# Optimization experiments

Measured on AMD Instinct MI355X. Metric: run time of the kernel, lower is better.

Reference implementation:

```python
import jax, jax.numpy as jnp
import numpy as np

KERNEL = 7          # kernel_size
DIL = 1             # dilation
PAD = 3             # padding (same output size for k=7, d=1, s=1)
STRIDE = 1


def setup_inputs() -> dict:
    key = jax.random.key(0)
    x = jax.random.normal(key, (4, 256, 64, 64), dtype=jnp.float32)
    return {"x": x}


def reference(x):
    b, c, h, w = x.shape
    k2 = KERNEL * KERNEL
    # im2col / F.unfold equivalent: (b, c*k2, h_out, w_out), features ordered
    # (channel, kh, kw) exactly like torch.nn.functional.unfold.
    patches = jax.lax.conv_general_dilated_patches(
        x,
        filter_shape=(KERNEL, KERNEL),
        window_strides=(STRIDE, STRIDE),
        padding=[(PAD, PAD), (PAD, PAD)],
        rhs_dilation=(DIL, DIL),
    )
    ho, wo = patches.shape[2], patches.shape[3]
    p = patches.reshape(b, c, k2, ho, wo)          # (b, c, k2, h, w)
    center = p[:, :, k2 // 2]                      # (b, c, h, w) center of window
    # per-pixel similarity of each window element to the center, over channels
    sim = jnp.einsum('bckhw,bchw->bkhw', p, center)  # (b, k2, h, w)
    attn = jax.nn.softmax(sim, axis=1)               # softmax over window dim
    # weighted sum of window features
    out = jnp.einsum('bkhw,bckhw->bchw', attn, p)    # (b, c, h, w)
    return out
```

## Files before the change

### kernel.cpp

```cpp
#include <hip/hip_runtime.h>

typedef float f4 __attribute__((ext_vector_type(4)));
typedef _Float16 h2 __attribute__((ext_vector_type(2)));

#define Hdim 64
#define Wdim 64
#define Cdim 256
#define HW (Hdim * Wdim)

__device__ __forceinline__ float fdot2f(h2 a, h2 b, float c) {
#if __has_builtin(__builtin_amdgcn_fdot2)
    return __builtin_amdgcn_fdot2(a, b, c, false);
#else
    float d;
    asm("v_dot2_f32_f16 %0, %1, %2, %3" : "=v"(d) : "v"(a), "v"(b), "v"(c));
    return d;
#endif
}

__global__ __launch_bounds__(512) void pack_kernel(const float* __restrict__ x,
                                                   float* __restrict__ pw)
{
    const int tid = blockIdx.x * 512 + threadIdx.x;
    const int wq = tid & 15;
    const int h  = (tid >> 4) & 63;
    const int cp = (tid >> 10) & 127;
    const int b  = tid >> 17;
    const float* s0 = x + ((size_t)b * Cdim + 2 * cp) * HW + h * 64 + wq * 4;
    f4 v0 = *(const f4*)s0;
    f4 v1 = *(const f4*)(s0 + HW);
    f4 ov;
    #pragma unroll
    for (int p = 0; p < 4; ++p) {
        h2 o;
        o[0] = (_Float16)v0[p];
        o[1] = (_Float16)v1[p];
        ov[p] = __builtin_bit_cast(float, o);
    }
    *(f4*)(pw + ((size_t)b * 128 + cp) * HW + h * 64 + wq * 4) = ov;
}

__global__ __launch_bounds__(512, 2) void selfattn_f16(const float* __restrict__ pwf,
                                                       float* __restrict__ out)
{
    const int bid = blockIdx.x;
    const int k   = bid & 7;
    const int seq = bid >> 3;
    const int b   = k >> 1;
    const int h   = (k & 1) * 32 + (seq >> 1);
    const int wbase = (seq & 1) * 32;
    const int t = threadIdx.x;

    __shared__ float simRed[49][32];
    __shared__ __align__(16) h2 attnH[49][32];
    __shared__ float redBuf[7][32];
    __shared__ float psumBuf[7][32];

    const float* pw = pwf + (size_t)b * (128 * HW);

    {
        const int w4 = t & 7;
        const int cp = (t >> 3) & 7;
        const int dy = t >> 6;
        const int lw0 = w4 * 4;
        const int w0g = wbase + lw0;

        if (dy < 7) {
            float sim[7][4];
            #pragma unroll
            for (int dx = 0; dx < 7; ++dx)
                #pragma unroll
                for (int p = 0; p < 4; ++p) sim[dx][p] = 0.f;

            const int row = h + dy - 3;
            if (row >= 0 && row < Hdim) {
                const bool hasL = (w0g != 0);
                const bool hasR = (w0g != 60);
                const float* xr = pw + (size_t)cp * HW + row * 64;
                const float* xc = pw + (size_t)cp * HW + h   * 64;
                for (int i = 0; i < 16; ++i) {
                    float fw[12];
                    if (hasL) {
                        f4 v = *(const f4*)(xr + w0g - 4);
                        fw[0]=v.x; fw[1]=v.y; fw[2]=v.z; fw[3]=v.w;
                    } else { fw[0]=0.f; fw[1]=0.f; fw[2]=0.f; fw[3]=0.f; }
                    {
                        f4 v = *(const f4*)(xr + w0g);
                        fw[4]=v.x; fw[5]=v.y; fw[6]=v.z; fw[7]=v.w;
                    }
                    if (hasR) {
                        f4 v = *(const f4*)(xr + w0g + 4);
                        fw[8]=v.x; fw[9]=v.y; fw[10]=v.z; fw[11]=v.w;
                    } else { fw[8]=0.f; fw[9]=0.f; fw[10]=0.f; fw[11]=0.f; }
                    f4 cen = *(const f4*)(xc + w0g);
                    h2 f2[12], cen2[4];
                    #pragma unroll
                    for (int j = 0; j < 12; ++j) f2[j] = __builtin_bit_cast(h2, fw[j]);
                    #pragma unroll
                    for (int p = 0; p < 4; ++p) cen2[p] = __builtin_bit_cast(h2, cen[p]);
                    #pragma unroll
                    for (int dx = 0; dx < 7; ++dx)
                        #pragma unroll
                        for (int p = 0; p < 4; ++p)
                            sim[dx][p] = fdot2f(cen2[p], f2[dx + p + 1], sim[dx][p]);
                    xr += 8 * HW;
                    xc += 8 * HW;
                }
            }
            #pragma unroll
            for (int dx = 0; dx < 7; ++dx)
                #pragma unroll
                for (int p = 0; p < 4; ++p) {
                    float v = sim[dx][p];
                    v += __shfl_xor(v, 8);
                    v += __shfl_xor(v, 16);
                    v += __shfl_xor(v, 32);
                    sim[dx][p] = v;
                }
            if (cp == 0) {
                #pragma unroll
                for (int dx = 0; dx < 7; ++dx)
                    *(f4*)&simRed[dy * 7 + dx][lw0] = *(const f4*)sim[dx];
            }
        }
    }
    __syncthreads();

    {
        const int w  = t & 31;
        const int kc = t >> 5;
        float sred[7], e[7];
        if (kc < 7) {
            float lmax = -3.0e38f;
            #pragma unroll
            for (int jj = 0; jj < 7; ++jj) {
                float s = simRed[kc * 7 + jj][w];
                sred[jj] = s;
                lmax = fmaxf(lmax, s);
            }
            redBuf[kc][w] = lmax;
        }
        __syncthreads();
        if (kc < 7) {
            float m = redBuf[0][w];
            #pragma unroll
            for (int q = 1; q < 7; ++q) m = fmaxf(m, redBuf[q][w]);
            float ps = 0.f;
            #pragma unroll
            for (int jj = 0; jj < 7; ++jj) {
                e[jj] = __expf(sred[jj] - m);
                ps += e[jj];
            }
            psumBuf[kc][w] = ps;
        }
        __syncthreads();
        if (kc < 7) {
            float l = psumBuf[0][w];
            #pragma unroll
            for (int q = 1; q < 7; ++q) l += psumBuf[q][w];
            float rinv = 1.0f / l;
            #pragma unroll
            for (int jj = 0; jj < 7; ++jj) {
                _Float16 ah = (_Float16)(e[jj] * rinv);
                h2 av; av[0] = ah; av[1] = ah;
                attnH[kc * 7 + jj][w] = av;
            }
        }
    }
    __syncthreads();

    {
        const int w4 = t & 7;
        const int ci = t >> 3;
        const int lw0 = w4 * 4;
        const int w0g = wbase + lw0;
        const bool hasL = (w0g != 0);
        const bool hasR = (w0g != 60);

        h2 acc2[2][4];
        #pragma unroll
        for (int pr = 0; pr < 2; ++pr)
            #pragma unroll
            for (int p = 0; p < 4; ++p) { acc2[pr][p][0] = (_Float16)0; acc2[pr][p][1] = (_Float16)0; }

        for (int dy = 0; dy < 7; ++dy) {
            const int row = h + dy - 3;
            if (row < 0 || row >= Hdim) continue;
            h2 a2[7][4];
            #pragma unroll
            for (int dx = 0; dx < 7; ++dx) {
                f4 v = *(const f4*)&attnH[dy * 7 + dx][lw0];
                #pragma unroll
                for (int p = 0; p < 4; ++p) a2[dx][p] = __builtin_bit_cast(h2, v[p]);
            }
            #pragma unroll
            for (int pr = 0; pr < 2; ++pr) {
                const float* xr = pw + (size_t)(2 * ci + pr) * HW + row * 64;
                float fw[12];
                if (hasL) {
                    f4 v = *(const f4*)(xr + w0g - 4);
                    fw[0]=v.x; fw[1]=v.y; fw[2]=v.z; fw[3]=v.w;
                } else { fw[0]=0.f; fw[1]=0.f; fw[2]=0.f; fw[3]=0.f; }
                {
                    f4 v = *(const f4*)(xr + w0g);
                    fw[4]=v.x; fw[5]=v.y; fw[6]=v.z; fw[7]=v.w;
                }
                if (hasR) {
                    f4 v = *(const f4*)(xr + w0g + 4);
                    fw[8]=v.x; fw[9]=v.y; fw[10]=v.z; fw[11]=v.w;
                } else { fw[8]=0.f; fw[9]=0.f; fw[10]=0.f; fw[11]=0.f; }
                h2 f2[12];
                #pragma unroll
                for (int j = 0; j < 12; ++j) f2[j] = __builtin_bit_cast(h2, fw[j]);
                #pragma unroll
                for (int dx = 0; dx < 7; ++dx)
                    #pragma unroll
                    for (int p = 0; p < 4; ++p)
                        acc2[pr][p] += a2[dx][p] * f2[dx + p + 1];
            }
        }

        float* ob = out + (size_t)b * (Cdim * HW) + h * Wdim + w0g;
        #pragma unroll
        for (int pr = 0; pr < 2; ++pr) {
            f4 o0, o1;
            #pragma unroll
            for (int p = 0; p < 4; ++p) {
                o0[p] = (float)acc2[pr][p][0];
                o1[p] = (float)acc2[pr][p][1];
            }
            const int c0 = 4 * ci + 2 * pr;
            *(f4*)(ob + (size_t)c0 * HW)       = o0;
            *(f4*)(ob + (size_t)(c0 + 1) * HW) = o1;
        }
    }
}

__global__ __launch_bounds__(512, 2) void selfattn_fb(const float* __restrict__ x,
                                                      float* __restrict__ out)
{
    const int bid = blockIdx.x;
    const int k   = bid & 7;
    const int seq = bid >> 3;
    const int b   = k >> 1;
    const int h   = (k & 1) * 32 + (seq >> 1);
    const int wbase = (seq & 1) * 32;
    const int t = threadIdx.x;

    __shared__ float simRed[49][32];
    __shared__ float attnBuf[49][32];
    __shared__ float redBuf[7][32];
    __shared__ float psumBuf[7][32];

    const float* xb = x + (size_t)b * (Cdim * HW);

    {
        const int w4 = t & 7;
        const int cp = (t >> 3) & 7;
        const int dy = t >> 6;
        const int lw0 = w4 * 4;
        const int w0g = wbase + lw0;

        if (dy < 7) {
            float sim[7][4];
            #pragma unroll
            for (int dx = 0; dx < 7; ++dx)
                #pragma unroll
                for (int p = 0; p < 4; ++p) sim[dx][p] = 0.f;

            const int row = h + dy - 3;
            if (row >= 0 && row < Hdim) {
                const bool hasL = (w0g != 0);
                const bool hasR = (w0g != 60);
                const float* xrA = xb + (size_t)cp * HW + row * Wdim;
                const float* xcA = xb + (size_t)cp * HW + h   * Wdim;
                const float* xrB = xrA + (size_t)128 * HW;
                const float* xcB = xcA + (size_t)128 * HW;
                #pragma unroll 2
                for (int i = 0; i < 16; ++i) {
                    float fA[12], fB[12];
                    if (hasL) {
                        f4 v = *(const f4*)(xrA + w0g - 4);
                        fA[0]=v.x; fA[1]=v.y; fA[2]=v.z; fA[3]=v.w;
                    } else { fA[0]=0.f; fA[1]=0.f; fA[2]=0.f; fA[3]=0.f; }
                    {
                        f4 v = *(const f4*)(xrA + w0g);
                        fA[4]=v.x; fA[5]=v.y; fA[6]=v.z; fA[7]=v.w;
                    }
                    if (hasR) {
                        f4 v = *(const f4*)(xrA + w0g + 4);
                        fA[8]=v.x; fA[9]=v.y; fA[10]=v.z; fA[11]=v.w;
                    } else { fA[8]=0.f; fA[9]=0.f; fA[10]=0.f; fA[11]=0.f; }
                    if (hasL) {
                        f4 v = *(const f4*)(xrB + w0g - 4);
                        fB[0]=v.x; fB[1]=v.y; fB[2]=v.z; fB[3]=v.w;
                    } else { fB[0]=0.f; fB[1]=0.f; fB[2]=0.f; fB[3]=0.f; }
                    {
                        f4 v = *(const f4*)(xrB + w0g);
                        fB[4]=v.x; fB[5]=v.y; fB[6]=v.z; fB[7]=v.w;
                    }
                    if (hasR) {
                        f4 v = *(const f4*)(xrB + w0g + 4);
                        fB[8]=v.x; fB[9]=v.y; fB[10]=v.z; fB[11]=v.w;
                    } else { fB[8]=0.f; fB[9]=0.f; fB[10]=0.f; fB[11]=0.f; }
                    f4 cenA = *(const f4*)(xcA + w0g);
                    f4 cenB = *(const f4*)(xcB + w0g);
                    #pragma unroll
                    for (int dx = 0; dx < 7; ++dx)
                        #pragma unroll
                        for (int p = 0; p < 4; ++p)
                            sim[dx][p] += cenA[p] * fA[dx + p + 1]
                                        + cenB[p] * fB[dx + p + 1];
                    xrA += 8 * HW;  xcA += 8 * HW;
                    xrB += 8 * HW;  xcB += 8 * HW;
                }
            }
            #pragma unroll
            for (int dx = 0; dx < 7; ++dx)
                #pragma unroll
                for (int p = 0; p < 4; ++p) {
                    float v = sim[dx][p];
                    v += __shfl_xor(v, 8);
                    v += __shfl_xor(v, 16);
                    v += __shfl_xor(v, 32);
                    sim[dx][p] = v;
                }
            if (cp == 0) {
                #pragma unroll
                for (int dx = 0; dx < 7; ++dx)
                    *(f4*)&simRed[dy * 7 + dx][lw0] = *(const f4*)sim[dx];
            }
        }
    }
    __syncthreads();

    {
        const int w  = t & 31;
        const int kc = t >> 5;
        float sred[7], e[7];
        if (kc < 7) {
            float lmax = -3.0e38f;
            #pragma unroll
            for (int jj = 0; jj < 7; ++jj) {
                float s = simRed[kc * 7 + jj][w];
                sred[jj] = s;
                lmax = fmaxf(lmax, s);
            }
            redBuf[kc][w] = lmax;
        }
        __syncthreads();
        if (kc < 7) {
            float m = redBuf[0][w];
            #pragma unroll
            for (int q = 1; q < 7; ++q) m = fmaxf(m, redBuf[q][w]);
            float ps = 0.f;
            #pragma unroll
            for (int jj = 0; jj < 7; ++jj) {
                e[jj] = __expf(sred[jj] - m);
                ps += e[jj];
            }
            psumBuf[kc][w] = ps;
        }
        __syncthreads();
        if (kc < 7) {
            float l = psumBuf[0][w];
            #pragma unroll
            for (int q = 1; q < 7; ++q) l += psumBuf[q][w];
            float rinv = 1.0f / l;
            #pragma unroll
            for (int jj = 0; jj < 7; ++jj)
                attnBuf[kc * 7 + jj][w] = e[jj] * rinv;
        }
    }
    __syncthreads();

    {
        const int w4 = t & 7;
        const int ci = t >> 3;
        const int lw0 = w4 * 4;
        const int w0g = wbase + lw0;
        const int c0 = ci * 4;
        const bool hasL = (w0g != 0);
        const bool hasR = (w0g != 60);

        float acc[4][4];
        #pragma unroll
        for (int ch = 0; ch < 4; ++ch)
            #pragma unroll
            for (int p = 0; p < 4; ++p) acc[ch][p] = 0.f;

        for (int dy = 0; dy < 7; ++dy) {
            const int row = h + dy - 3;
            if (row < 0 || row >= Hdim) continue;
            float a[7][4];
            #pragma unroll
            for (int dx = 0; dx < 7; ++dx) {
                f4 v = *(const f4*)&attnBuf[dy * 7 + dx][lw0];
                a[dx][0]=v.x; a[dx][1]=v.y; a[dx][2]=v.z; a[dx][3]=v.w;
            }
            const float* xr = xb + (size_t)c0 * HW + row * Wdim;
            #pragma unroll
            for (int ch = 0; ch < 4; ++ch) {
                float fw[12];
                if (hasL) {
                    f4 v = *(const f4*)(xr + w0g - 4);
                    fw[0]=v.x; fw[1]=v.y; fw[2]=v.z; fw[3]=v.w;
                } else { fw[0]=0.f; fw[1]=0.f; fw[2]=0.f; fw[3]=0.f; }
                {
                    f4 v = *(const f4*)(xr + w0g);
                    fw[4]=v.x; fw[5]=v.y; fw[6]=v.z; fw[7]=v.w;
                }
                if (hasR) {
                    f4 v = *(const f4*)(xr + w0g + 4);
                    fw[8]=v.x; fw[9]=v.y; fw[10]=v.z; fw[11]=v.w;
                } else { fw[8]=0.f; fw[9]=0.f; fw[10]=0.f; fw[11]=0.f; }
                #pragma unroll
                for (int dx = 0; dx < 7; ++dx)
                    #pragma unroll
                    for (int p = 0; p < 4; ++p)
                        acc[ch][p] += a[dx][p] * fw[dx + p + 1];
                xr += HW;
            }
        }

        float* ob = out + (size_t)b * (Cdim * HW) + h * Wdim + wbase;
        #pragma unroll
        for (int ch = 0; ch < 4; ++ch)
            *(f4*)(ob + (size_t)(c0 + ch) * HW + lw0) = *(const f4*)acc[ch];
    }
}

extern "C" void kernel_launch(void* const* d_in, const int* in_sizes, int n_in,
                              void* d_out, int out_size, void* d_ws, size_t ws_size,
                              hipStream_t stream)
{
    const float* x = (const float*)d_in[0];
    float* out = (float*)d_out;
    const size_t need = (size_t)4 * 128 * HW * 4;
    if (ws_size >= need) {
        float* pw = (float*)d_ws;
        pack_kernel<<<dim3(1024), 512, 0, stream>>>(x, pw);
        selfattn_f16<<<dim3(512), 512, 0, stream>>>(pw, out);
    } else {
        selfattn_fb<<<dim3(512), 512, 0, stream>>>(x, out);
    }
}
```

Baseline: 33.21 us.

## Process two output rows per block to reuse shared neighbor rows

Each block now handles a pair of adjacent output rows with 1024 threads instead of one row with 512. The 8 input rows covering both 7-row windows are loaded once and used for both rows' similarity and weighted-sum stages. This roughly halves the redundant global loads of neighboring rows. Channels are split across two wave groups, and their partial sums are combined in shared memory. In exchange the grid shrinks to 256 blocks, which lowers the number of blocks per CU, and register pressure rises from the dual accumulators.

```diff
diff --git a/kernel.cpp b/kernel.cpp
--- a/kernel.cpp
+++ b/kernel.cpp
@@ -40,162 +40,54 @@
     *(f4*)(pw + ((size_t)b * 128 + cp) * HW + h * 64 + wq * 4) = ov;
 }
 
-__global__ __launch_bounds__(512, 2) void selfattn_f16(const float* __restrict__ pwf,
+__global__ __launch_bounds__(1024) void selfattn_hpair(const float* __restrict__ pwf,
                                                        float* __restrict__ out)
 {
     const int bid = blockIdx.x;
     const int k   = bid & 7;
     const int seq = bid >> 3;
     const int b   = k >> 1;
-    const int h   = (k & 1) * 32 + (seq >> 1);
+    const int hh  = k & 1;
+    const int hp  = seq >> 1;
+    const int h0  = hh * 32 + hp * 2;
+    const int h1  = h0 + 1;
     const int wbase = (seq & 1) * 32;
     const int t = threadIdx.x;
 
-    __shared__ float simRed[49][32];
-    __shared__ __align__(16) h2 attnH[49][32];
-    __shared__ float redBuf[7][32];
-    __shared__ float psumBuf[7][32];
+    __shared__ float simPart[2][2][49][32];
+    __shared__ __align__(16) h2 attnH[2][49][32];
+    __shared__ float redBuf[2][7][32];
+    __shared__ float psumBuf[2][7][32];
 
     const float* pw = pwf + (size_t)b * (128 * HW);
 
     {
+        const int wave = t >> 6;
+        const int r    = wave & 7;
+        const int g    = wave >> 3;
         const int w4 = t & 7;
         const int cp = (t >> 3) & 7;
-        const int dy = t >> 6;
         const int lw0 = w4 * 4;
         const int w0g = wbase + lw0;
-
-        if (dy < 7) {
-            float sim[7][4];
-            #pragma unroll
-            for (int dx = 0; dx < 7; ++dx)
-                #pragma unroll
-                for (int p = 0; p < 4; ++p) sim[dx][p] = 0.f;
-
-            const int row = h + dy - 3;
-            if (row >= 0 && row < Hdim) {
-                const bool hasL = (w0g != 0);
-                const bool hasR = (w0g != 60);
-                const float* xr = pw + (size_t)cp * HW + row * 64;
-                const float* xc = pw + (size_t)cp * HW + h   * 64;
-                for (int i = 0; i < 16; ++i) {
-                    float fw[12];
-                    if (hasL) {
-                        f4 v = *(const f4*)(xr + w0g - 4);
-                        fw[0]=v.x; fw[1]=v.y; fw[2]=v.z; fw[3]=v.w;
-                    } else { fw[0]=0.f; fw[1]=0.f; fw[2]=0.f; fw[3]=0.f; }
-                    {
-                        f4 v = *(const f4*)(xr + w0g);
-                        fw[4]=v.x; fw[5]=v.y; fw[6]=v.z; fw[7]=v.w;
-                    }
-                    if (hasR) {
-                        f4 v = *(const f4*)(xr + w0g + 4);
-                        fw[8]=v.x; fw[9]=v.y; fw[10]=v.z; fw[11]=v.w;
-                    } else { fw[8]=0.f; fw[9]=0.f; fw[10]=0.f; fw[11]=0.f; }
-                    f4 cen = *(const f4*)(xc + w0g);
-                    h2 f2[12], cen2[4];
-                    #pragma unroll
-                    for (int j = 0; j < 12; ++j) f2[j] = __builtin_bit_cast(h2, fw[j]);
-                    #pragma unroll
-                    for (int p = 0; p < 4; ++p) cen2[p] = __builtin_bit_cast(h2, cen[p]);
-                    #pragma unroll
-                    for (int dx = 0; dx < 7; ++dx)
-                        #pragma unroll
-                        for (int p = 0; p < 4; ++p)
-                            sim[dx][p] = fdot2f(cen2[p], f2[dx + p + 1], sim[dx][p]);
-                    xr += 8 * HW;
-                    xc += 8 * HW;
-                }
-            }
-            #pragma unroll
-            for (int dx = 0; dx < 7; ++dx)
-                #pragma unroll
-                for (int p = 0; p < 4; ++p) {
-                    float v = sim[dx][p];
-                    v += __shfl_xor(v, 8);
-                    v += __shfl_xor(v, 16);
-                    v += __shfl_xor(v, 32);
-                    sim[dx][p] = v;
-                }
-            if (cp == 0) {
-                #pragma unroll
-                for (int dx = 0; dx < 7; ++dx)
-                    *(f4*)&simRed[dy * 7 + dx][lw0] = *(const f4*)sim[dx];
-            }
-        }
-    }
-    __syncthreads();
-
-    {
-        const int w  = t & 31;
-        const int kc = t >> 5;
-        float sred[7], e[7];
-        if (kc < 7) {
-            float lmax = -3.0e38f;
-            #pragma unroll
-            for (int jj = 0; jj < 7; ++jj) {
-                float s = simRed[kc * 7 + jj][w];
-                sred[jj] = s;
-                lmax = fmaxf(lmax, s);
-            }
-            redBuf[kc][w] = lmax;
-        }
-        __syncthreads();
-        if (kc < 7) {
-            float m = redBuf[0][w];
-            #pragma unroll
-            for (int q = 1; q < 7; ++q) m = fmaxf(m, redBuf[q][w]);
-            float ps = 0.f;
-            #pragma unroll
-            for (int jj = 0; jj < 7; ++jj) {
-                e[jj] = __expf(sred[jj] - m);
-                ps += e[jj];
-            }
-            psumBuf[kc][w] = ps;
-        }
-        __syncthreads();
-        if (kc < 7) {
-            float l = psumBuf[0][w];
-            #pragma unroll
-            for (int q = 1; q < 7; ++q) l += psumBuf[q][w];
-            float rinv = 1.0f / l;
-            #pragma unroll
-            for (int jj = 0; jj < 7; ++jj) {
-                _Float16 ah = (_Float16)(e[jj] * rinv);
-                h2 av; av[0] = ah; av[1] = ah;
-                attnH[kc * 7 + jj][w] = av;
-            }
-        }
-    }
-    __syncthreads();
-
-    {
-        const int w4 = t & 7;
-        const int ci = t >> 3;
-        const int lw0 = w4 * 4;
-        const int w0g = wbase + lw0;
-        const bool hasL = (w0g != 0);
-        const bool hasR = (w0g != 60);
-
-        h2 acc2[2][4];
+        const int gr = h0 - 3 + r;
+        const bool grok = (gr >= 0 && gr < Hdim);
+        const bool use0 = (r <= 6);
+        const bool use1 = (r >= 1);
+
+        float sim0[7][4], sim1[7][4];
         #pragma unroll
-        for (int pr = 0; pr < 2; ++pr)
-            #pragma unroll
-            for (int p = 0; p < 4; ++p) { acc2[pr][p][0] = (_Float16)0; acc2[pr][p][1] = (_Float16)0; }
-
-        for (int dy = 0; dy < 7; ++dy) {
-            const int row = h + dy - 3;
-            if (row < 0 || row >= Hdim) continue;
-            h2 a2[7][4];
-            #pragma unroll
-            for (int dx = 0; dx < 7; ++dx) {
-                f4 v = *(const f4*)&attnH[dy * 7 + dx][lw0];
-                #pragma unroll
-                for (int p = 0; p < 4; ++p) a2[dx][p] = __builtin_bit_cast(h2, v[p]);
-            }
-            #pragma unroll
-            for (int pr = 0; pr < 2; ++pr) {
-                const float* xr = pw + (size_t)(2 * ci + pr) * HW + row * 64;
+        for (int dx = 0; dx < 7; ++dx)
+            #pragma unroll
+            for (int p = 0; p < 4; ++p) { sim0[dx][p] = 0.f; sim1[dx][p] = 0.f; }
+
+        if (grok) {
+            const bool hasL = (w0g != 0);
+            const bool hasR = (w0g != 60);
+            const float* xr  = pw + (size_t)(g * 8 + cp) * HW + gr * 64;
+            const float* xc0 = pw + (size_t)(g * 8 + cp) * HW + h0 * 64;
+            const float* xc1 = xc0 + 64;
+            #pragma unroll 2
+            for (int i = 0; i < 8; ++i) {
                 float fw[12];
                 if (hasL) {
                     f4 v = *(const f4*)(xr + w0g - 4);
@@ -211,28 +103,189 @@
                 } else { fw[8]=0.f; fw[9]=0.f; fw[10]=0.f; fw[11]=0.f; }
                 h2 f2[12];
                 #pragma unroll
-                for (int j = 0; j < 12; ++j) f2[j] = __builtin_bit_cast(h2, fw[j]);
+                for (int jj = 0; jj < 12; ++jj) f2[jj] = __builtin_bit_cast(h2, fw[jj]);
+                if (use0) {
+                    f4 c0 = *(const f4*)(xc0 + w0g);
+                    h2 c02[4];
+                    #pragma unroll
+                    for (int p = 0; p < 4; ++p) c02[p] = __builtin_bit_cast(h2, c0[p]);
+                    #pragma unroll
+                    for (int dx = 0; dx < 7; ++dx)
+                        #pragma unroll
+                        for (int p = 0; p < 4; ++p)
+                            sim0[dx][p] = fdot2f(c02[p], f2[dx + p + 1], sim0[dx][p]);
+                }
+                if (use1) {
+                    f4 c1 = *(const f4*)(xc1 + w0g);
+                    h2 c12[4];
+                    #pragma unroll
+                    for (int p = 0; p < 4; ++p) c12[p] = __builtin_bit_cast(h2, c1[p]);
+                    #pragma unroll
+                    for (int dx = 0; dx < 7; ++dx)
+                        #pragma unroll
+                        for (int p = 0; p < 4; ++p)
+                            sim1[dx][p] = fdot2f(c12[p], f2[dx + p + 1], sim1[dx][p]);
+                }
+                xr  += 16 * HW;
+                xc0 += 16 * HW;
+                xc1 += 16 * HW;
+            }
+        }
+        if (use0) {
+            #pragma unroll
+            for (int dx = 0; dx < 7; ++dx)
+                #pragma unroll
+                for (int p = 0; p < 4; ++p) {
+                    float v = sim0[dx][p];
+                    v += __shfl_xor(v, 8);
+                    v += __shfl_xor(v, 16);
+                    v += __shfl_xor(v, 32);
+                    sim0[dx][p] = v;
+                }
+        }
+        if (use1) {
+            #pragma unroll
+            for (int dx = 0; dx < 7; ++dx)
+                #pragma unroll
+                for (int p = 0; p < 4; ++p) {
+                    float v = sim1[dx][p];
+                    v += __shfl_xor(v, 8);
+                    v += __shfl_xor(v, 16);
+                    v += __shfl_xor(v, 32);
+                    sim1[dx][p] = v;
+                }
+        }
+        if (cp == 0) {
+            if (use0) {
                 #pragma unroll
                 for (int dx = 0; dx < 7; ++dx)
+                    *(f4*)&simPart[0][g][r * 7 + dx][lw0] = *(const f4*)sim0[dx];
+            }
+            if (use1) {
+                #pragma unroll
+                for (int dx = 0; dx < 7; ++dx)
+                    *(f4*)&simPart[1][g][(r - 1) * 7 + dx][lw0] = *(const f4*)sim1[dx];
+            }
+        }
+    }
+    __syncthreads();
+
+    {
+        const int hsel = t >> 9;
+        const int tt = t & 511;
+        const int w  = tt & 31;
+        const int kc = tt >> 5;
+        float sred[7], e[7];
+        if (kc < 7) {
+            float lmax = -3.0e38f;
+            #pragma unroll
+            for (int jj = 0; jj < 7; ++jj) {
+                const int idx = kc * 7 + jj;
+                float s = simPart[hsel][0][idx][w] + simPart[hsel][1][idx][w];
+                sred[jj] = s;
+                lmax = fmaxf(lmax, s);
+            }
+            redBuf[hsel][kc][w] = lmax;
+        }
+        __syncthreads();
+        if (kc < 7) {
+            float m = redBuf[hsel][0][w];
+            #pragma unroll
+            for (int q = 1; q < 7; ++q) m = fmaxf(m, redBuf[hsel][q][w]);
+            float ps = 0.f;
+            #pragma unroll
+            for (int jj = 0; jj < 7; ++jj) {
+                e[jj] = __expf(sred[jj] - m);
+                ps += e[jj];
+            }
+            psumBuf[hsel][kc][w] = ps;
+        }
+        __syncthreads();
+        if (kc < 7) {
+            float l = psumBuf[hsel][0][w];
+            #pragma unroll
+            for (int q = 1; q < 7; ++q) l += psumBuf[hsel][q][w];
+            float rinv = 1.0f / l;
+            #pragma unroll
+            for (int jj = 0; jj < 7; ++jj) {
+                _Float16 ah = (_Float16)(e[jj] * rinv);
+                h2 av; av[0] = ah; av[1] = ah;
+                attnH[hsel][kc * 7 + jj][w] = av;
+            }
+        }
+    }
+    __syncthreads();
+
+    {
+        const int w4 = t & 7;
+        const int ci = t >> 3;
+        const int lw0 = w4 * 4;
+        const int w0g = wbase + lw0;
+        const bool hasL = (w0g != 0);
+        const bool hasR = (w0g != 60);
+
+        h2 acc0[4], acc1[4];
+        #pragma unroll
+        for (int p = 0; p < 4; ++p) {
+            acc0[p][0] = (_Float16)0; acc0[p][1] = (_Float16)0;
+            acc1[p][0] = (_Float16)0; acc1[p][1] = (_Float16)0;
+        }
+
+        const float* xbase = pw + (size_t)ci * HW;
+        #pragma unroll 2
+        for (int rr = 0; rr < 8; ++rr) {
+            const int grow = h0 - 3 + rr;
+            if (grow < 0 || grow >= Hdim) continue;
+            const float* xr = xbase + grow * 64;
+            float fw[12];
+            if (hasL) {
+                f4 v = *(const f4*)(xr + w0g - 4);
+                fw[0]=v.x; fw[1]=v.y; fw[2]=v.z; fw[3]=v.w;
+            } else { fw[0]=0.f; fw[1]=0.f; fw[2]=0.f; fw[3]=0.f; }
+            {
+                f4 v = *(const f4*)(xr + w0g);
+                fw[4]=v.x; fw[5]=v.y; fw[6]=v.z; fw[7]=v.w;
+            }
+            if (hasR) {
+                f4 v = *(const f4*)(xr + w0g + 4);
+                fw[8]=v.x; fw[9]=v.y; fw[10]=v.z; fw[11]=v.w;
+            } else { fw[8]=0.f; fw[9]=0.f; fw[10]=0.f; fw[11]=0.f; }
+            h2 f2[12];
+            #pragma unroll
+            for (int jj = 0; jj < 12; ++jj) f2[jj] = __builtin_bit_cast(h2, fw[jj]);
+            if (rr <= 6) {
+                #pragma unroll
+                for (int dx = 0; dx < 7; ++dx) {
+                    f4 av = *(const f4*)&attnH[0][rr * 7 + dx][lw0];
                     #pragma unroll
                     for (int p = 0; p < 4; ++p)
-                        acc2[pr][p] += a2[dx][p] * f2[dx + p + 1];
-            }
-        }
-
-        float* ob = out + (size_t)b * (Cdim * HW) + h * Wdim + w0g;
+                        acc0[p] += __builtin_bit_cast(h2, av[p]) * f2[dx + p + 1];
+                }
+            }
+            if (rr >= 1) {
+                #pragma unroll
+                for (int dx = 0; dx < 7; ++dx) {
+                    f4 av = *(const f4*)&attnH[1][(rr - 1) * 7 + dx][lw0];
+                    #pragma unroll
+                    for (int p = 0; p < 4; ++p)
+                        acc1[p] += __builtin_bit_cast(h2, av[p]) * f2[dx + p + 1];
+                }
+            }
+        }
+
+        float* ob = out + (size_t)b * (Cdim * HW) + w0g;
+        f4 o00, o01, o10, o11;
         #pragma unroll
-        for (int pr = 0; pr < 2; ++pr) {
-            f4 o0, o1;
-            #pragma unroll
-            for (int p = 0; p < 4; ++p) {
-                o0[p] = (float)acc2[pr][p][0];
-                o1[p] = (float)acc2[pr][p][1];
-            }
-            const int c0 = 4 * ci + 2 * pr;
-            *(f4*)(ob + (size_t)c0 * HW)       = o0;
-            *(f4*)(ob + (size_t)(c0 + 1) * HW) = o1;
-        }
+        for (int p = 0; p < 4; ++p) {
+            o00[p] = (float)acc0[p][0];
+            o01[p] = (float)acc0[p][1];
+            o10[p] = (float)acc1[p][0];
+            o11[p] = (float)acc1[p][1];
+        }
+        *(f4*)(ob + (size_t)(2 * ci) * HW     + h0 * 64) = o00;
+        *(f4*)(ob + (size_t)(2 * ci + 1) * HW + h0 * 64) = o01;
+        *(f4*)(ob + (size_t)(2 * ci) * HW     + h1 * 64) = o10;
+        *(f4*)(ob + (size_t)(2 * ci + 1) * HW + h1 * 64) = o11;
     }
 }
 
@@ -440,7 +493,7 @@
     if (ws_size >= need) {
         float* pw = (float*)d_ws;
         pack_kernel<<<dim3(1024), 512, 0, stream>>>(x, pw);
-        selfattn_f16<<<dim3(512), 512, 0, stream>>>(pw, out);
+        selfattn_hpair<<<dim3(256), 1024, 0, stream>>>(pw, out);
     } else {
         selfattn_fb<<<dim3(512), 512, 0, stream>>>(x, out);
     }
```

Result: slower. 34.58 us (+4.1%).

## Split fused attention kernel into similarity and output kernels with global attn buffer

Applied to the files above, without the earlier changes.

The fused f16 kernel is split into two launches. ka_sim computes the 49-tap softmax weights and writes them to a workspace buffer. kb_out reloads them into LDS and computes the weighted sum over half the channel pairs per block, doubling the grid to 1024 blocks. The goal is more parallelism and lower register pressure in the output phase, at the cost of an extra launch, a global round-trip for the weights, and redundant halo loads across the two channel halves.

```diff
diff --git a/kernel.cpp b/kernel.cpp
--- a/kernel.cpp
+++ b/kernel.cpp
@@ -40,19 +40,19 @@
     *(f4*)(pw + ((size_t)b * 128 + cp) * HW + h * 64 + wq * 4) = ov;
 }
 
-__global__ __launch_bounds__(512, 2) void selfattn_f16(const float* __restrict__ pwf,
-                                                       float* __restrict__ out)
+__global__ __launch_bounds__(512, 2) void ka_sim(const float* __restrict__ pwf,
+                                                 float* __restrict__ attnG)
 {
     const int bid = blockIdx.x;
     const int k   = bid & 7;
     const int seq = bid >> 3;
     const int b   = k >> 1;
     const int h   = (k & 1) * 32 + (seq >> 1);
-    const int wbase = (seq & 1) * 32;
+    const int whalf = seq & 1;
+    const int wbase = whalf * 32;
     const int t = threadIdx.x;
 
     __shared__ float simRed[49][32];
-    __shared__ __align__(16) h2 attnH[49][32];
     __shared__ float redBuf[7][32];
     __shared__ float psumBuf[7][32];
 
@@ -159,12 +159,41 @@
             #pragma unroll
             for (int q = 1; q < 7; ++q) l += psumBuf[q][w];
             float rinv = 1.0f / l;
+            float* ag = attnG + (size_t)(((b * 64 + h) * 2 + whalf) * 49) * 32;
             #pragma unroll
             for (int jj = 0; jj < 7; ++jj) {
                 _Float16 ah = (_Float16)(e[jj] * rinv);
                 h2 av; av[0] = ah; av[1] = ah;
-                attnH[kc * 7 + jj][w] = av;
-            }
+                ag[(kc * 7 + jj) * 32 + w] = __builtin_bit_cast(float, av);
+            }
+        }
+    }
+}
+
+__global__ __launch_bounds__(512) void kb_out(const float* __restrict__ pwf,
+                                              const float* __restrict__ attnG,
+                                              float* __restrict__ out)
+{
+    const int bid = blockIdx.x;
+    const int k   = bid & 7;
+    const int seq = bid >> 3;
+    const int b   = k >> 1;
+    const int h   = (k & 1) * 32 + (seq >> 2);
+    const int whalf = (seq >> 1) & 1;
+    const int chalf = seq & 1;
+    const int wbase = whalf * 32;
+    const int t = threadIdx.x;
+
+    __shared__ __align__(16) h2 attnH[49][32];
+
+    const float* pw = pwf + (size_t)b * (128 * HW);
+
+    {
+        const float* ag = attnG + (size_t)(((b * 64 + h) * 2 + whalf) * 49) * 32;
+        if (t < 392) {
+            const int kk = t >> 3;
+            const int wq = t & 7;
+            *(f4*)&attnH[kk][wq * 4] = *(const f4*)(ag + kk * 32 + wq * 4);
         }
     }
     __syncthreads();
@@ -172,16 +201,15 @@
     {
         const int w4 = t & 7;
         const int ci = t >> 3;
+        const int pair = chalf * 64 + ci;
         const int lw0 = w4 * 4;
         const int w0g = wbase + lw0;
         const bool hasL = (w0g != 0);
         const bool hasR = (w0g != 60);
 
-        h2 acc2[2][4];
+        h2 acc2[4];
         #pragma unroll
-        for (int pr = 0; pr < 2; ++pr)
-            #pragma unroll
-            for (int p = 0; p < 4; ++p) { acc2[pr][p][0] = (_Float16)0; acc2[pr][p][1] = (_Float16)0; }
+        for (int p = 0; p < 4; ++p) { acc2[p][0] = (_Float16)0; acc2[p][1] = (_Float16)0; }
 
         for (int dy = 0; dy < 7; ++dy) {
             const int row = h + dy - 3;
@@ -193,46 +221,39 @@
                 #pragma unroll
                 for (int p = 0; p < 4; ++p) a2[dx][p] = __builtin_bit_cast(h2, v[p]);
             }
-            #pragma unroll
-            for (int pr = 0; pr < 2; ++pr) {
-                const float* xr = pw + (size_t)(2 * ci + pr) * HW + row * 64;
-                float fw[12];
-                if (hasL) {
-                    f4 v = *(const f4*)(xr + w0g - 4);
-                    fw[0]=v.x; fw[1]=v.y; fw[2]=v.z; fw[3]=v.w;
-                } else { fw[0]=0.f; fw[1]=0.f; fw[2]=0.f; fw[3]=0.f; }
-                {
-                    f4 v = *(const f4*)(xr + w0g);
-                    fw[4]=v.x; fw[5]=v.y; fw[6]=v.z; fw[7]=v.w;
-                }
-                if (hasR) {
-                    f4 v = *(const f4*)(xr + w0g + 4);
-                    fw[8]=v.x; fw[9]=v.y; fw[10]=v.z; fw[11]=v.w;
-                } else { fw[8]=0.f; fw[9]=0.f; fw[10]=0.f; fw[11]=0.f; }
-                h2 f2[12];
-                #pragma unroll
-                for (int j = 0; j < 12; ++j) f2[j] = __builtin_bit_cast(h2, fw[j]);
-                #pragma unroll
-                for (int dx = 0; dx < 7; ++dx)
-                    #pragma unroll
-                    for (int p = 0; p < 4; ++p)
-                        acc2[pr][p] += a2[dx][p] * f2[dx + p + 1];
-            }
+            const float* xr = pw + (size_t)pair * HW + row * 64;
+            float fw[12];
+            if (hasL) {
+                f4 v = *(const f4*)(xr + w0g - 4);
+                fw[0]=v.x; fw[1]=v.y; fw[2]=v.z; fw[3]=v.w;
+            } else { fw[0]=0.f; fw[1]=0.f; fw[2]=0.f; fw[3]=0.f; }
+            {
+                f4 v = *(const f4*)(xr + w0g);
+                fw[4]=v.x; fw[5]=v.y; fw[6]=v.z; fw[7]=v.w;
+            }
+            if (hasR) {
+                f4 v = *(const f4*)(xr + w0g + 4);
+                fw[8]=v.x; fw[9]=v.y; fw[10]=v.z; fw[11]=v.w;
+            } else { fw[8]=0.f; fw[9]=0.f; fw[10]=0.f; fw[11]=0.f; }
+            h2 f2[12];
+            #pragma unroll
+            for (int j = 0; j < 12; ++j) f2[j] = __builtin_bit_cast(h2, fw[j]);
+            #pragma unroll
+            for (int dx = 0; dx < 7; ++dx)
+                #pragma unroll
+                for (int p = 0; p < 4; ++p)
+                    acc2[p] += a2[dx][p] * f2[dx + p + 1];
         }
 
         float* ob = out + (size_t)b * (Cdim * HW) + h * Wdim + w0g;
+        f4 o0, o1;
         #pragma unroll
-        for (int pr = 0; pr < 2; ++pr) {
-            f4 o0, o1;
-            #pragma unroll
-            for (int p = 0; p < 4; ++p) {
-                o0[p] = (float)acc2[pr][p][0];
-                o1[p] = (float)acc2[pr][p][1];
-            }
-            const int c0 = 4 * ci + 2 * pr;
-            *(f4*)(ob + (size_t)c0 * HW)       = o0;
-            *(f4*)(ob + (size_t)(c0 + 1) * HW) = o1;
-        }
+        for (int p = 0; p < 4; ++p) {
+            o0[p] = (float)acc2[p][0];
+            o1[p] = (float)acc2[p][1];
+        }
+        *(f4*)(ob + (size_t)(2 * pair) * HW)     = o0;
+        *(f4*)(ob + (size_t)(2 * pair + 1) * HW) = o1;
     }
 }
 
@@ -436,11 +457,15 @@
 {
     const float* x = (const float*)d_in[0];
     float* out = (float*)d_out;
-    const size_t need = (size_t)4 * 128 * HW * 4;
+    const size_t pwFloats = (size_t)4 * 128 * HW;
+    const size_t attnFloats = (size_t)512 * 49 * 32;
+    const size_t need = (pwFloats + attnFloats) * 4;
     if (ws_size >= need) {
         float* pw = (float*)d_ws;
+        float* attnG = pw + pwFloats;
         pack_kernel<<<dim3(1024), 512, 0, stream>>>(x, pw);
-        selfattn_f16<<<dim3(512), 512, 0, stream>>>(pw, out);
+        ka_sim<<<dim3(512), 512, 0, stream>>>(pw, attnG);
+        kb_out<<<dim3(1024), 512, 0, stream>>>(pw, attnG, out);
     } else {
         selfattn_fb<<<dim3(512), 512, 0, stream>>>(x, out);
     }
```

Result: slower. 35.84 us (+7.9%).
